# Performance work log

Hardware: AMD Instinct MI355X
Metric: run time of the kernel (lower is better)

## Reference

```python
import jax, jax.numpy as jnp
import numpy as np
from jax import lax

DIM = 256
NUM_HEADS = 8
HEAD_DIM = DIM // NUM_HEADS
DN = ('NCHW', 'OIHW', 'NCHW')


def _dsconv(x, dw, dwb, pw, pwb):
    # depthwise 3x3 (groups = C) then pointwise 1x1
    C = x.shape[1]
    y = lax.conv_general_dilated(x, dw, (1, 1), 'SAME',
                                 dimension_numbers=DN,
                                 feature_group_count=C)
    y = y + dwb[None, :, None, None]
    y = lax.conv_general_dilated(y, pw, (1, 1), 'SAME', dimension_numbers=DN)
    return y + pwb[None, :, None, None]


def _to_heads(x):
    # (B, C, H, W) -> (B, nh, HW, hd)
    B, C, H, W = x.shape
    return x.reshape(B, NUM_HEADS, HEAD_DIM, H * W).transpose(0, 1, 3, 2)


def setup_inputs() -> dict:
    key = jax.random.key(0)
    ks = jax.random.split(key, 14)
    B, H, W = 2, 64, 64
    inp = {
        'x': jax.random.normal(ks[0], (B, DIM, H, W), jnp.float32),
        'ctx': jax.random.normal(ks[1], (B, DIM, H, W), jnp.float32),
    }
    i = 2
    for name in ('q', 'k', 'v'):
        inp[f'{name}_dw'] = jax.random.normal(ks[i], (DIM, 1, 3, 3), jnp.float32) * 0.05; i += 1
        inp[f'{name}_dwb'] = jnp.zeros((DIM,), jnp.float32)
        inp[f'{name}_pw'] = jax.random.normal(ks[i], (DIM, DIM, 1, 1), jnp.float32) * 0.05; i += 1
        inp[f'{name}_pwb'] = jnp.zeros((DIM,), jnp.float32)
    return inp


def reference(x, ctx,
              q_dw, q_dwb, q_pw, q_pwb,
              k_dw, k_dwb, k_pw, k_pwb,
              v_dw, v_dwb, v_pw, v_pwb):
    B, C, H, W = x.shape
    scale = HEAD_DIM ** 0.5
    q = _to_heads(_dsconv(x, q_dw, q_dwb, q_pw, q_pwb))    # (B, nh, HW, hd)
    k = _to_heads(_dsconv(ctx, k_dw, k_dwb, k_pw, k_pwb))
    v = _to_heads(_dsconv(ctx, v_dw, v_dwb, v_pw, v_pwb))
    attn = jnp.einsum('bnqd,bnkd->bnqk', q, k) / scale      # (B, nh, HW, HW)
    attn = jax.nn.softmax(attn, axis=-1)
    out = jnp.einsum('bnqk,bnkd->bnqd', attn, v)            # (B, nh, HW, hd)
    out = out.transpose(0, 1, 3, 2).reshape(B, DIM, H * W)  # (B, dim, HW)
    return out
```

## Files before the change

kernel.cpp:

```cpp
#include <hip/hip_runtime.h>
#include <hip/hip_bf16.h>


#define HW 4096
#define CDIM 256
#define SCALE_LOG2E 0.2550348543f

typedef short bf16x8 __attribute__((ext_vector_type(8)));
typedef float f32x2 __attribute__((ext_vector_type(2)));
typedef float f32x4 __attribute__((ext_vector_type(4)));
typedef float f32x16 __attribute__((ext_vector_type(16)));

__device__ inline unsigned short f2bf(float f) {
  unsigned u = __float_as_uint(f);
  u = (u + 0x7fffu + ((u >> 16) & 1u)) >> 16;
  return (unsigned short)u;
}

__device__ inline unsigned cvtpk(float lo, float hi) {
  unsigned r;
  asm("v_cvt_pk_bf16_f32 %0, %1, %2" : "=v"(r) : "v"(lo), "v"(hi));
  return r;
}

__device__ inline float fexp2(float x) {
#if __has_builtin(__builtin_amdgcn_exp2f)
  return __builtin_amdgcn_exp2f(x);
#else
  return exp2f(x);
#endif
}

__device__ inline void plswap(unsigned& a, unsigned& b) {
#if __has_builtin(__builtin_amdgcn_permlane32_swap)
  auto r = __builtin_amdgcn_permlane32_swap((int)a, (int)b, false, false);
  a = (unsigned)r[0];
  b = (unsigned)r[1];
#else
  unsigned as = __shfl_xor((int)a, 32), bs = __shfl_xor((int)b, 32);
  bool hi = (threadIdx.x & 32) != 0;
  unsigned na = hi ? bs : a;
  unsigned nb = hi ? b : as;
  a = na; b = nb;
#endif
}

__global__ __launch_bounds__(256) void dw_all(
    const float* __restrict__ x, const float* __restrict__ ctx,
    const float* __restrict__ qdw, const float* __restrict__ qdwb,
    const float* __restrict__ kdw, const float* __restrict__ kdwb,
    const float* __restrict__ vdw, const float* __restrict__ vdwb,
    unsigned short* __restrict__ tq, unsigned short* __restrict__ tk,
    unsigned short* __restrict__ tv) {
  int gid = blockIdx.x * 256 + threadIdx.x;
  int pass = gid >> 19;
  int r = gid & 524287;
  int q4 = r & 1023;
  int plane = r >> 10;
  int c = plane & 255;
  int w0 = (q4 & 15) * 4, h = q4 >> 4;
  const float* src = (pass ? ctx : x) + (size_t)plane * HW;

  float e[3][6];
#pragma unroll
  for (int kh = 0; kh < 3; ++kh) {
    int hh = h + kh - 1;
    if (hh < 0 || hh > 63) {
#pragma unroll
      for (int j = 0; j < 6; ++j) e[kh][j] = 0.f;
    } else {
      const float* row = src + hh * 64 + w0;
      float4 m = *(const float4*)row;
      e[kh][0] = (w0 > 0) ? row[-1] : 0.f;
      e[kh][1] = m.x; e[kh][2] = m.y; e[kh][3] = m.z; e[kh][4] = m.w;
      e[kh][5] = (w0 < 60) ? row[4] : 0.f;
    }
  }
  size_t obase = (size_t)plane * HW + h * 64 + w0;
  if (pass == 0) {
    const float* wc = qdw + c * 9;
    float bv = qdwb[c];
    float a0 = bv, a1 = bv, a2 = bv, a3 = bv;
#pragma unroll
    for (int kh = 0; kh < 3; ++kh) {
      float w_0 = wc[kh * 3], w_1 = wc[kh * 3 + 1], w_2 = wc[kh * 3 + 2];
      a0 += w_0 * e[kh][0] + w_1 * e[kh][1] + w_2 * e[kh][2];
      a1 += w_0 * e[kh][1] + w_1 * e[kh][2] + w_2 * e[kh][3];
      a2 += w_0 * e[kh][2] + w_1 * e[kh][3] + w_2 * e[kh][4];
      a3 += w_0 * e[kh][3] + w_1 * e[kh][4] + w_2 * e[kh][5];
    }
    *(ushort4*)(tq + obase) = make_ushort4(f2bf(a0), f2bf(a1), f2bf(a2), f2bf(a3));
  } else {
    const float* wk = kdw + c * 9;
    const float* wvv = vdw + c * 9;
    float bk = kdwb[c], bv2 = vdwb[c];
    float k0 = bk, k1 = bk, k2 = bk, k3 = bk;
    float v0 = bv2, v1 = bv2, v2 = bv2, v3 = bv2;
#pragma unroll
    for (int kh = 0; kh < 3; ++kh) {
      float kw0 = wk[kh * 3], kw1 = wk[kh * 3 + 1], kw2 = wk[kh * 3 + 2];
      float vw0 = wvv[kh * 3], vw1 = wvv[kh * 3 + 1], vw2 = wvv[kh * 3 + 2];
      k0 += kw0 * e[kh][0] + kw1 * e[kh][1] + kw2 * e[kh][2];
      k1 += kw0 * e[kh][1] + kw1 * e[kh][2] + kw2 * e[kh][3];
      k2 += kw0 * e[kh][2] + kw1 * e[kh][3] + kw2 * e[kh][4];
      k3 += kw0 * e[kh][3] + kw1 * e[kh][4] + kw2 * e[kh][5];
      v0 += vw0 * e[kh][0] + vw1 * e[kh][1] + vw2 * e[kh][2];
      v1 += vw0 * e[kh][1] + vw1 * e[kh][2] + vw2 * e[kh][3];
      v2 += vw0 * e[kh][2] + vw1 * e[kh][3] + vw2 * e[kh][4];
      v3 += vw0 * e[kh][3] + vw1 * e[kh][4] + vw2 * e[kh][5];
    }
    *(ushort4*)(tk + obase) = make_ushort4(f2bf(k0), f2bf(k1), f2bf(k2), f2bf(k3));
    *(ushort4*)(tv + obase) = make_ushort4(f2bf(v0), f2bf(v1), f2bf(v2), f2bf(v3));
  }
}

__global__ __launch_bounds__(256) void pw_all(
    const unsigned short* __restrict__ tq, const unsigned short* __restrict__ tk,
    const unsigned short* __restrict__ tv,
    const float* __restrict__ qw, const float* __restrict__ qbs,
    const float* __restrict__ kw, const float* __restrict__ kbs,
    const float* __restrict__ vw, const float* __restrict__ vbs,
    unsigned short* __restrict__ Qc, unsigned short* __restrict__ Kc,
    unsigned short* __restrict__ Vc) {
  __shared__ __align__(16) unsigned char Bs[64 * 512];
  int tt = blockIdx.x >> 9;
  int bid = blockIdx.x & 511;
  const unsigned short* t = tt == 0 ? tq : (tt == 1 ? tk : tv);
  const float* w = tt == 0 ? qw : (tt == 1 ? kw : vw);
  const float* bias = tt == 0 ? qbs : (tt == 1 ? kbs : vbs);
  unsigned short* out = tt == 0 ? Qc : (tt == 1 ? Kc : Vc);
  float oscale = tt == 0 ? SCALE_LOG2E : 1.0f;

  int pt = bid & 63, cot = (bid >> 6) & 3, bb = bid >> 8;
  int p0 = pt * 64, co0 = cot * 64;
  int tid = threadIdx.x;
  int wv = tid >> 6, l = tid & 63, lq = l & 15, lg = l >> 4;

  bf16x8 af[8];
  {
    const float* wr = w + (size_t)(co0 + wv * 16 + lq) * 256;
#pragma unroll
    for (int kt = 0; kt < 8; ++kt) {
      float4 a = *(const float4*)(wr + kt * 32 + lg * 8);
      float4 bq = *(const float4*)(wr + kt * 32 + lg * 8 + 4);
      union { unsigned u[4]; bf16x8 v; } cv;
      cv.u[0] = cvtpk(a.x, a.y);  cv.u[1] = cvtpk(a.z, a.w);
      cv.u[2] = cvtpk(bq.x, bq.y); cv.u[3] = cvtpk(bq.z, bq.w);
      af[kt] = cv.v;
    }
  }
  {
    int cb = tid >> 3, po = tid & 7;
    const unsigned short* src = t + (size_t)bb * (CDIM * HW) + (size_t)(cb * 8) * HW + p0 + po * 8;
    uint4 r[8];
#pragma unroll
    for (int i = 0; i < 8; ++i) r[i] = *(const uint4*)(src + (size_t)i * HW);
#pragma unroll
    for (int jj = 0; jj < 8; ++jj) {
      uint4 o;
#pragma unroll
      for (int ww = 0; ww < 4; ++ww) {
        unsigned a = ((const unsigned*)&r[2 * ww])[jj >> 1];
        unsigned b = ((const unsigned*)&r[2 * ww + 1])[jj >> 1];
        unsigned lo = (jj & 1) ? (a >> 16) : (a & 0xffffu);
        unsigned hi = (jj & 1) ? (b & 0xffff0000u) : (b << 16);
        (&o.x)[ww] = lo | hi;
      }
      int p = po * 8 + jj;
      int swz = ((p ^ (p >> 3)) & 7) << 4;
      *(uint4*)(Bs + p * 512 + ((cb * 16) ^ swz)) = o;
    }
  }
  __syncthreads();
  f32x4 acc[4] = {};
#pragma unroll
  for (int nt = 0; nt < 4; ++nt) {
    int p = nt * 16 + lq;
    int swz = ((p ^ (p >> 3)) & 7) << 4;
    const unsigned char* Bp = Bs + p * 512;
#pragma unroll
    for (int kt = 0; kt < 8; ++kt) {
      bf16x8 bf = *(const bf16x8*)(Bp + ((kt * 64 + lg * 16) ^ swz));
      acc[nt] = __builtin_amdgcn_mfma_f32_16x16x32_bf16(af[kt], bf, acc[nt], 0, 0, 0);
    }
  }
  if (tt < 2) {
    int co = co0 + wv * 16 + lg * 4;
    int d0 = co & 31;
    float b0 = bias[co], b1 = bias[co + 1], b2 = bias[co + 2], b3 = bias[co + 3];
    size_t rowb = (size_t)(bb * 8 + (co >> 5)) * HW;
#pragma unroll
    for (int nt = 0; nt < 4; ++nt) {
      int p = p0 + nt * 16 + lq;
      ushort4 pk = make_ushort4(f2bf((acc[nt][0] + b0) * oscale),
                                f2bf((acc[nt][1] + b1) * oscale),
                                f2bf((acc[nt][2] + b2) * oscale),
                                f2bf((acc[nt][3] + b3) * oscale));
      *(ushort4*)(out + (rowb + p) * 32 + d0) = pk;
    }
  } else {
    int cob = co0 + wv * 16 + lg * 4;
#pragma unroll
    for (int r = 0; r < 4; ++r) {
      float bv = bias[cob + r];
      size_t rb = (size_t)bb * (CDIM * HW) + (size_t)(cob + r) * HW + p0;
#pragma unroll
      for (int nt = 0; nt < 4; ++nt)
        out[rb + nt * 16 + lq] = f2bf(acc[nt][r] + bv);
    }
  }
}

__global__ __launch_bounds__(256, 3) void attn_kernel(
    const unsigned short* __restrict__ Qt, const unsigned short* __restrict__ Kt,
    const unsigned short* __restrict__ Vn, float* __restrict__ out) {
  __shared__ __align__(16) unsigned char lds[20480];
  int bid0 = blockIdx.x;
  int bid = (bid0 & 7) * 128 + (bid0 >> 3);
  int qb = bid & 63, bh = bid >> 6;
  int b = bh >> 3, n = bh & 7;
  int tid = threadIdx.x;
  int l = tid & 63, ks = tid >> 6;
  int lq = l & 31, hi = l >> 5;

  const unsigned short* Qg = Qt + (size_t)bh * (HW * 32);
  const unsigned short* Kg = Kt + (size_t)bh * (HW * 32);
  const unsigned short* Vg = Vn + (size_t)(b * CDIM + n * 32) * HW;

  int q0 = qb * 64;
  bf16x8 qa0 = *(const bf16x8*)(Qg + (size_t)(q0 + lq) * 32 + hi * 8);
  bf16x8 qa1 = *(const bf16x8*)(Qg + (size_t)(q0 + lq) * 32 + 16 + hi * 8);
  bf16x8 qB0 = *(const bf16x8*)(Qg + (size_t)(q0 + 32 + lq) * 32 + hi * 8);
  bf16x8 qB1 = *(const bf16x8*)(Qg + (size_t)(q0 + 32 + lq) * 32 + 16 + hi * 8);

  f32x16 Oa = {}, Ob = {}, ZZ = {};
  float psa = 0.f, psb = 0.f;

  unsigned char* Kl = lds + ks * 5120;
  unsigned char* Vl = Kl + 2560;
  int u0i = l, u1i = l + 64;
  unsigned char* Kw0 = Kl + (u0i >> 2) * 80 + (u0i & 3) * 16;
  unsigned char* Kw1 = Kl + (u1i >> 2) * 80 + (u1i & 3) * 16;
  unsigned char* Vw0 = Vl + (u0i >> 2) * 80 + (u0i & 3) * 16;
  unsigned char* Vw1 = Vl + (u1i >> 2) * 80 + (u1i & 3) * 16;
  const uint4* Ks4 = (const uint4*)Kg + (size_t)ks * 4096;
  const unsigned short* Vs0 = Vg + (size_t)(u0i >> 2) * HW + ks * 1024 + (u0i & 3) * 8;
  const unsigned short* Vs1 = Vg + (size_t)(u1i >> 2) * HW + ks * 1024 + (u1i & 3) * 8;

  uint4 ks0 = Ks4[u0i], ks1 = Ks4[u1i];
  uint4 vs0 = *(const uint4*)Vs0, vs1 = *(const uint4*)Vs1;
  *(uint4*)Kw0 = ks0; *(uint4*)Kw1 = ks1;
  *(uint4*)Vw0 = vs0; *(uint4*)Vw1 = vs1;

  const unsigned char* Kr = Kl + lq * 80 + hi * 16;
  const unsigned char* Vr = Vl + lq * 80 + hi * 16;

  auto subtile = [&](bf16x8 kfa, bf16x8 kfb, bf16x8 va, bf16x8 vb,
                     bf16x8 qf0, bf16x8 qf1, f32x16& O, float& ps) {
    __builtin_amdgcn_s_setprio(1);
    f32x16 st = __builtin_amdgcn_mfma_f32_32x32x16_bf16(kfa, qf0, ZZ, 0, 0, 0);
    st = __builtin_amdgcn_mfma_f32_32x32x16_bf16(kfb, qf1, st, 0, 0, 0);
    __builtin_amdgcn_s_setprio(0);
    float p[16];
#pragma unroll
    for (int r = 0; r < 16; ++r) p[r] = fexp2(st[r]);
    f32x2 s0 = (f32x2){p[0], p[1]} + (f32x2){p[2], p[3]};
    f32x2 s1 = (f32x2){p[4], p[5]} + (f32x2){p[6], p[7]};
    f32x2 s2 = (f32x2){p[8], p[9]} + (f32x2){p[10], p[11]};
    f32x2 s3 = (f32x2){p[12], p[13]} + (f32x2){p[14], p[15]};
    f32x2 s4 = (s0 + s1) + (s2 + s3);
    ps += s4[0] + s4[1];
    unsigned u0 = cvtpk(p[0], p[1]),  u1 = cvtpk(p[2], p[3]);
    unsigned u2 = cvtpk(p[4], p[5]),  u3 = cvtpk(p[6], p[7]);
    unsigned u4 = cvtpk(p[8], p[9]),  u5 = cvtpk(p[10], p[11]);
    unsigned u6 = cvtpk(p[12], p[13]), u7 = cvtpk(p[14], p[15]);
    plswap(u0, u2);
    plswap(u1, u3);
    plswap(u4, u6);
    plswap(u5, u7);
    union { unsigned w[4]; bf16x8 v; } X1, X2;
    X1.w[0] = u0; X1.w[1] = u1; X1.w[2] = u2; X1.w[3] = u3;
    X2.w[0] = u4; X2.w[1] = u5; X2.w[2] = u6; X2.w[3] = u7;
    __builtin_amdgcn_s_setprio(1);
    O = __builtin_amdgcn_mfma_f32_32x32x16_bf16(va, X1.v, O, 0, 0, 0);
    O = __builtin_amdgcn_mfma_f32_32x32x16_bf16(vb, X2.v, O, 0, 0, 0);
    __builtin_amdgcn_s_setprio(0);
  };

#pragma unroll 1
  for (int c = 0; c < 32; ++c) {
    bf16x8 kfa = *(const bf16x8*)(Kr);
    bf16x8 kfb = *(const bf16x8*)(Kr + 32);
    bf16x8 va  = *(const bf16x8*)(Vr);
    bf16x8 vb  = *(const bf16x8*)(Vr + 32);
    if (c < 31) {
      ks0 = Ks4[(c + 1) * 128 + u0i];
      ks1 = Ks4[(c + 1) * 128 + u1i];
      vs0 = *(const uint4*)(Vs0 + (c + 1) * 32);
      vs1 = *(const uint4*)(Vs1 + (c + 1) * 32);
    }
    subtile(kfa, kfb, va, vb, qa0, qa1, Oa, psa);
    subtile(kfa, kfb, va, vb, qB0, qB1, Ob, psb);
    if (c < 31) {
      *(uint4*)Kw0 = ks0; *(uint4*)Kw1 = ks1;
      *(uint4*)Vw0 = vs0; *(uint4*)Vw1 = vs1;
    }
  }

  psa += __shfl_xor(psa, 32);
  psb += __shfl_xor(psb, 32);
  __syncthreads();
  float* MO = (float*)lds;
  float* MS = (float*)lds + 4224;
  const int SET = 2112, SUB = 1056;

  if (ks == 1 || ks == 3) {
    int s = (ks == 3);
#pragma unroll
    for (int r = 0; r < 16; ++r) {
      int d = (r & 3) + 8 * (r >> 2) + 4 * hi;
      MO[s * SET + d * 33 + lq] = Oa[r];
      MO[s * SET + SUB + d * 33 + lq] = Ob[r];
    }
    if (hi == 0) {
      MS[s * 128 + lq] = psa;
      MS[s * 128 + 32 + lq] = psb;
    }
  }
  __syncthreads();
  if (ks == 0 || ks == 2) {
    int s = (ks == 2);
#pragma unroll
    for (int r = 0; r < 16; ++r) {
      int d = (r & 3) + 8 * (r >> 2) + 4 * hi;
      Oa[r] += MO[s * SET + d * 33 + lq];
      Ob[r] += MO[s * SET + SUB + d * 33 + lq];
    }
    psa += MS[s * 128 + lq];
    psb += MS[s * 128 + 32 + lq];
  }
  __syncthreads();
  if (ks == 2) {
#pragma unroll
    for (int r = 0; r < 16; ++r) {
      int d = (r & 3) + 8 * (r >> 2) + 4 * hi;
      MO[d * 33 + lq] = Oa[r];
      MO[SUB + d * 33 + lq] = Ob[r];
    }
    if (hi == 0) {
      MS[lq] = psa;
      MS[32 + lq] = psb;
    }
  }
  __syncthreads();
  if (ks == 0) {
    float rva, rvb;
    {
#pragma unroll
      for (int r = 0; r < 16; ++r) {
        int d = (r & 3) + 8 * (r >> 2) + 4 * hi;
        Oa[r] += MO[d * 33 + lq];
        Ob[r] += MO[SUB + d * 33 + lq];
      }
      rva = 1.0f / (psa + MS[lq]);
      rvb = 1.0f / (psb + MS[32 + lq]);
    }
    size_t ob = ((size_t)(b * CDIM) + n * 32) * HW;
#pragma unroll
    for (int r = 0; r < 16; ++r) {
      int d = (r & 3) + 8 * (r >> 2) + 4 * hi;
      out[ob + (size_t)d * HW + q0 + lq] = Oa[r] * rva;
      out[ob + (size_t)d * HW + q0 + 32 + lq] = Ob[r] * rvb;
    }
  }
}

extern "C" void kernel_launch(void* const* d_in, const int* in_sizes, int n_in,
                              void* d_out, int out_size, void* d_ws, size_t ws_size,
                              hipStream_t stream) {
  const float* x   = (const float*)d_in[0];
  const float* ctx = (const float*)d_in[1];
  const float* q_dw  = (const float*)d_in[2];
  const float* q_dwb = (const float*)d_in[3];
  const float* q_pw  = (const float*)d_in[4];
  const float* q_pwb = (const float*)d_in[5];
  const float* k_dw  = (const float*)d_in[6];
  const float* k_dwb = (const float*)d_in[7];
  const float* k_pw  = (const float*)d_in[8];
  const float* k_pwb = (const float*)d_in[9];
  const float* v_dw  = (const float*)d_in[10];
  const float* v_dwb = (const float*)d_in[11];
  const float* v_pw  = (const float*)d_in[12];
  const float* v_pwb = (const float*)d_in[13];

  const size_t N = (size_t)2 * CDIM * HW;
  unsigned short* Qc = (unsigned short*)d_ws;
  unsigned short* Kc = Qc + N;
  unsigned short* Vc = Kc + N;
  unsigned short* tv = Vc + N;
  unsigned short* tq = (unsigned short*)d_out;
  unsigned short* tk = tq + N;

  dw_all<<<4096, 256, 0, stream>>>(x, ctx, q_dw, q_dwb, k_dw, k_dwb, v_dw, v_dwb,
                                   tq, tk, tv);
  pw_all<<<1536, 256, 0, stream>>>(tq, tk, tv, q_pw, q_pwb, k_pw, k_pwb,
                                   v_pw, v_pwb, Qc, Kc, Vc);
  attn_kernel<<<1024, 256, 0, stream>>>(Qc, Kc, Vc, (float*)d_out);
}
```

Before: 87.65 us.

## Double-buffer per-wave K/V LDS tiles with two-deep global prefetch in attention

```diff
diff --git a/kernel.cpp b/kernel.cpp
--- a/kernel.cpp
+++ b/kernel.cpp
@@ -214,7 +214,7 @@
 __global__ __launch_bounds__(256, 3) void attn_kernel(
     const unsigned short* __restrict__ Qt, const unsigned short* __restrict__ Kt,
     const unsigned short* __restrict__ Vn, float* __restrict__ out) {
-  __shared__ __align__(16) unsigned char lds[20480];
+  __shared__ __align__(16) unsigned char lds[40960];
   int bid0 = blockIdx.x;
   int bid = (bid0 & 7) * 128 + (bid0 >> 3);
   int qb = bid & 63, bh = bid >> 6;
@@ -236,24 +236,25 @@
   f32x16 Oa = {}, Ob = {}, ZZ = {};
   float psa = 0.f, psb = 0.f;
 
-  unsigned char* Kl = lds + ks * 5120;
-  unsigned char* Vl = Kl + 2560;
-  int u0i = l, u1i = l + 64;
-  unsigned char* Kw0 = Kl + (u0i >> 2) * 80 + (u0i & 3) * 16;
-  unsigned char* Kw1 = Kl + (u1i >> 2) * 80 + (u1i & 3) * 16;
-  unsigned char* Vw0 = Vl + (u0i >> 2) * 80 + (u0i & 3) * 16;
-  unsigned char* Vw1 = Vl + (u1i >> 2) * 80 + (u1i & 3) * 16;
+  unsigned char* E  = lds + ks * 10240;
+  unsigned char* Od = E + 5120;
+  int wr0 = (l >> 2) * 80 + (l & 3) * 16;
+  int rdK = lq * 80 + hi * 16;
+
   const uint4* Ks4 = (const uint4*)Kg + (size_t)ks * 4096;
-  const unsigned short* Vs0 = Vg + (size_t)(u0i >> 2) * HW + ks * 1024 + (u0i & 3) * 8;
-  const unsigned short* Vs1 = Vg + (size_t)(u1i >> 2) * HW + ks * 1024 + (u1i & 3) * 8;
-
-  uint4 ks0 = Ks4[u0i], ks1 = Ks4[u1i];
-  uint4 vs0 = *(const uint4*)Vs0, vs1 = *(const uint4*)Vs1;
-  *(uint4*)Kw0 = ks0; *(uint4*)Kw1 = ks1;
-  *(uint4*)Vw0 = vs0; *(uint4*)Vw1 = vs1;
-
-  const unsigned char* Kr = Kl + lq * 80 + hi * 16;
-  const unsigned char* Vr = Vl + lq * 80 + hi * 16;
+  const unsigned short* Vs0 = Vg + (size_t)(l >> 2) * HW + ks * 1024 + (l & 3) * 8;
+  const unsigned short* Vs1 = Vs0 + (size_t)16 * HW;
+
+  uint4 gk0 = Ks4[l], gk1 = Ks4[64 + l];
+  uint4 gv0 = *(const uint4*)Vs0, gv1 = *(const uint4*)Vs1;
+  *(uint4*)(E + wr0) = gk0;        *(uint4*)(E + wr0 + 1280) = gk1;
+  *(uint4*)(E + 2560 + wr0) = gv0; *(uint4*)(E + 2560 + wr0 + 1280) = gv1;
+  bf16x8 kfaA = *(const bf16x8*)(E + rdK);
+  bf16x8 kfbA = *(const bf16x8*)(E + rdK + 32);
+  bf16x8 vaA  = *(const bf16x8*)(E + 2560 + rdK);
+  bf16x8 vbA  = *(const bf16x8*)(E + 2560 + rdK + 32);
+  gk0 = Ks4[128 + l]; gk1 = Ks4[128 + 64 + l];
+  gv0 = *(const uint4*)(Vs0 + 32); gv1 = *(const uint4*)(Vs1 + 32);
 
   auto subtile = [&](bf16x8 kfa, bf16x8 kfb, bf16x8 va, bf16x8 vb,
                      bf16x8 qf0, bf16x8 qf1, f32x16& O, float& ps) {
@@ -288,23 +289,35 @@
   };
 
 #pragma unroll 1
-  for (int c = 0; c < 32; ++c) {
-    bf16x8 kfa = *(const bf16x8*)(Kr);
-    bf16x8 kfb = *(const bf16x8*)(Kr + 32);
-    bf16x8 va  = *(const bf16x8*)(Vr);
-    bf16x8 vb  = *(const bf16x8*)(Vr + 32);
-    if (c < 31) {
-      ks0 = Ks4[(c + 1) * 128 + u0i];
-      ks1 = Ks4[(c + 1) * 128 + u1i];
-      vs0 = *(const uint4*)(Vs0 + (c + 1) * 32);
-      vs1 = *(const uint4*)(Vs1 + (c + 1) * 32);
-    }
-    subtile(kfa, kfb, va, vb, qa0, qa1, Oa, psa);
-    subtile(kfa, kfb, va, vb, qB0, qB1, Ob, psb);
-    if (c < 31) {
-      *(uint4*)Kw0 = ks0; *(uint4*)Kw1 = ks1;
-      *(uint4*)Vw0 = vs0; *(uint4*)Vw1 = vs1;
-    }
+  for (int c = 0; c < 32; c += 2) {
+    *(uint4*)(Od + wr0) = gk0;        *(uint4*)(Od + wr0 + 1280) = gk1;
+    *(uint4*)(Od + 2560 + wr0) = gv0; *(uint4*)(Od + 2560 + wr0 + 1280) = gv1;
+    if (c + 2 < 32) {
+      gk0 = Ks4[(c + 2) * 128 + l]; gk1 = Ks4[(c + 2) * 128 + 64 + l];
+      gv0 = *(const uint4*)(Vs0 + (c + 2) * 32);
+      gv1 = *(const uint4*)(Vs1 + (c + 2) * 32);
+    }
+    bf16x8 kfaB = *(const bf16x8*)(Od + rdK);
+    bf16x8 kfbB = *(const bf16x8*)(Od + rdK + 32);
+    bf16x8 vaB  = *(const bf16x8*)(Od + 2560 + rdK);
+    bf16x8 vbB  = *(const bf16x8*)(Od + 2560 + rdK + 32);
+    subtile(kfaA, kfbA, vaA, vbA, qa0, qa1, Oa, psa);
+    subtile(kfaA, kfbA, vaA, vbA, qB0, qB1, Ob, psb);
+    if (c + 2 < 32) {
+      *(uint4*)(E + wr0) = gk0;        *(uint4*)(E + wr0 + 1280) = gk1;
+      *(uint4*)(E + 2560 + wr0) = gv0; *(uint4*)(E + 2560 + wr0 + 1280) = gv1;
+      if (c + 3 < 32) {
+        gk0 = Ks4[(c + 3) * 128 + l]; gk1 = Ks4[(c + 3) * 128 + 64 + l];
+        gv0 = *(const uint4*)(Vs0 + (c + 3) * 32);
+        gv1 = *(const uint4*)(Vs1 + (c + 3) * 32);
+      }
+      kfaA = *(const bf16x8*)(E + rdK);
+      kfbA = *(const bf16x8*)(E + rdK + 32);
+      vaA  = *(const bf16x8*)(E + 2560 + rdK);
+      vbA  = *(const bf16x8*)(E + 2560 + rdK + 32);
+    }
+    subtile(kfaB, kfbB, vaB, vbB, qa0, qa1, Oa, psa);
+    subtile(kfaB, kfbB, vaB, vbB, qB0, qB1, Ob, psb);
   }
 
   psa += __shfl_xor(psa, 32);
@@ -354,17 +367,14 @@
   }
   __syncthreads();
   if (ks == 0) {
-    float rva, rvb;
-    {
-#pragma unroll
-      for (int r = 0; r < 16; ++r) {
-        int d = (r & 3) + 8 * (r >> 2) + 4 * hi;
-        Oa[r] += MO[d * 33 + lq];
-        Ob[r] += MO[SUB + d * 33 + lq];
-      }
-      rva = 1.0f / (psa + MS[lq]);
-      rvb = 1.0f / (psb + MS[32 + lq]);
-    }
+#pragma unroll
+    for (int r = 0; r < 16; ++r) {
+      int d = (r & 3) + 8 * (r >> 2) + 4 * hi;
+      Oa[r] += MO[d * 33 + lq];
+      Ob[r] += MO[SUB + d * 33 + lq];
+    }
+    float rva = 1.0f / (psa + MS[lq]);
+    float rvb = 1.0f / (psb + MS[32 + lq]);
     size_t ob = ((size_t)(b * CDIM) + n * 32) * HW;
 #pragma unroll
     for (int r = 0; r < 16; ++r) {
```

Measured after the change: 88.06 us. About the same (+0.5%).

## Load K/V MFMA fragments directly from global with double-buffered registers

Applied to the files above, without the earlier changes.

```diff
diff --git a/kernel.cpp b/kernel.cpp
--- a/kernel.cpp
+++ b/kernel.cpp
@@ -214,7 +214,7 @@
 __global__ __launch_bounds__(256, 3) void attn_kernel(
     const unsigned short* __restrict__ Qt, const unsigned short* __restrict__ Kt,
     const unsigned short* __restrict__ Vn, float* __restrict__ out) {
-  __shared__ __align__(16) unsigned char lds[20480];
+  __shared__ __align__(16) float MOS[4736];
   int bid0 = blockIdx.x;
   int bid = (bid0 & 7) * 128 + (bid0 >> 3);
   int qb = bid & 63, bh = bid >> 6;
@@ -236,24 +236,17 @@
   f32x16 Oa = {}, Ob = {}, ZZ = {};
   float psa = 0.f, psb = 0.f;
 
-  unsigned char* Kl = lds + ks * 5120;
-  unsigned char* Vl = Kl + 2560;
-  int u0i = l, u1i = l + 64;
-  unsigned char* Kw0 = Kl + (u0i >> 2) * 80 + (u0i & 3) * 16;
-  unsigned char* Kw1 = Kl + (u1i >> 2) * 80 + (u1i & 3) * 16;
-  unsigned char* Vw0 = Vl + (u0i >> 2) * 80 + (u0i & 3) * 16;
-  unsigned char* Vw1 = Vl + (u1i >> 2) * 80 + (u1i & 3) * 16;
-  const uint4* Ks4 = (const uint4*)Kg + (size_t)ks * 4096;
-  const unsigned short* Vs0 = Vg + (size_t)(u0i >> 2) * HW + ks * 1024 + (u0i & 3) * 8;
-  const unsigned short* Vs1 = Vg + (size_t)(u1i >> 2) * HW + ks * 1024 + (u1i & 3) * 8;
-
-  uint4 ks0 = Ks4[u0i], ks1 = Ks4[u1i];
-  uint4 vs0 = *(const uint4*)Vs0, vs1 = *(const uint4*)Vs1;
-  *(uint4*)Kw0 = ks0; *(uint4*)Kw1 = ks1;
-  *(uint4*)Vw0 = vs0; *(uint4*)Vw1 = vs1;
-
-  const unsigned char* Kr = Kl + lq * 80 + hi * 16;
-  const unsigned char* Vr = Vl + lq * 80 + hi * 16;
+  const unsigned short* Kp = Kg + (size_t)(ks * 1024 + lq) * 32 + hi * 8;
+  const unsigned short* Vp = Vg + (size_t)lq * HW + ks * 1024 + hi * 8;
+
+  auto loadF = [&](int c, bf16x8& ka, bf16x8& kb, bf16x8& va, bf16x8& vb) {
+    const unsigned short* kp = Kp + (size_t)c * 1024;
+    ka = *(const bf16x8*)(kp);
+    kb = *(const bf16x8*)(kp + 16);
+    const unsigned short* vp = Vp + c * 32;
+    va = *(const bf16x8*)(vp);
+    vb = *(const bf16x8*)(vp + 16);
+  };
 
   auto subtile = [&](bf16x8 kfa, bf16x8 kfb, bf16x8 va, bf16x8 vb,
                      bf16x8 qf0, bf16x8 qf1, f32x16& O, float& ps) {
@@ -287,31 +280,25 @@
     __builtin_amdgcn_s_setprio(0);
   };
 
+  bf16x8 kaA, kbA, vaA, vbA, kaB, kbB, vaB, vbB;
+  loadF(0, kaA, kbA, vaA, vbA);
+  loadF(1, kaB, kbB, vaB, vbB);
+
 #pragma unroll 1
-  for (int c = 0; c < 32; ++c) {
-    bf16x8 kfa = *(const bf16x8*)(Kr);
-    bf16x8 kfb = *(const bf16x8*)(Kr + 32);
-    bf16x8 va  = *(const bf16x8*)(Vr);
-    bf16x8 vb  = *(const bf16x8*)(Vr + 32);
-    if (c < 31) {
-      ks0 = Ks4[(c + 1) * 128 + u0i];
-      ks1 = Ks4[(c + 1) * 128 + u1i];
-      vs0 = *(const uint4*)(Vs0 + (c + 1) * 32);
-      vs1 = *(const uint4*)(Vs1 + (c + 1) * 32);
-    }
-    subtile(kfa, kfb, va, vb, qa0, qa1, Oa, psa);
-    subtile(kfa, kfb, va, vb, qB0, qB1, Ob, psb);
-    if (c < 31) {
-      *(uint4*)Kw0 = ks0; *(uint4*)Kw1 = ks1;
-      *(uint4*)Vw0 = vs0; *(uint4*)Vw1 = vs1;
-    }
+  for (int c = 0; c < 32; c += 2) {
+    subtile(kaA, kbA, vaA, vbA, qa0, qa1, Oa, psa);
+    subtile(kaA, kbA, vaA, vbA, qB0, qB1, Ob, psb);
+    if (c + 2 < 32) loadF(c + 2, kaA, kbA, vaA, vbA);
+    subtile(kaB, kbB, vaB, vbB, qa0, qa1, Oa, psa);
+    subtile(kaB, kbB, vaB, vbB, qB0, qB1, Ob, psb);
+    if (c + 3 < 32) loadF(c + 3, kaB, kbB, vaB, vbB);
   }
 
   psa += __shfl_xor(psa, 32);
   psb += __shfl_xor(psb, 32);
   __syncthreads();
-  float* MO = (float*)lds;
-  float* MS = (float*)lds + 4224;
+  float* MO = MOS;
+  float* MS = MOS + 4224;
   const int SET = 2112, SUB = 1056;
 
   if (ks == 1 || ks == 3) {
@@ -354,17 +341,14 @@
   }
   __syncthreads();
   if (ks == 0) {
-    float rva, rvb;
-    {
-#pragma unroll
-      for (int r = 0; r < 16; ++r) {
-        int d = (r & 3) + 8 * (r >> 2) + 4 * hi;
-        Oa[r] += MO[d * 33 + lq];
-        Ob[r] += MO[SUB + d * 33 + lq];
-      }
-      rva = 1.0f / (psa + MS[lq]);
-      rvb = 1.0f / (psb + MS[32 + lq]);
-    }
+#pragma unroll
+    for (int r = 0; r < 16; ++r) {
+      int d = (r & 3) + 8 * (r >> 2) + 4 * hi;
+      Oa[r] += MO[d * 33 + lq];
+      Ob[r] += MO[SUB + d * 33 + lq];
+    }
+    float rva = 1.0f / (psa + MS[lq]);
+    float rvb = 1.0f / (psb + MS[32 + lq]);
     size_t ob = ((size_t)(b * CDIM) + n * 32) * HW;
 #pragma unroll
     for (int r = 0; r < 16; ++r) {
```

Result: no change. 86.64 us (-1.2%).
